# Performance work log

Hardware: AMD Instinct MI355X
Metric: run time of the kernel (lower is better)

Reference implementation:

```python
import jax, jax.numpy as jnp
import numpy as np

B, X, Y, Z = 1, 256, 256, 48
N_LABELS = 40  # static instance count (labels 1..N_LABELS; 0 = background)


def setup_inputs() -> dict:
    key = jax.random.key(0)
    # watershed integer label volume [B, 1, X, Y, Z]; stored as float32 (labels are
    # small non-negative integers, faithful to torch mask semantics under equality)
    mask = jax.random.randint(key, (B, 1, X, Y, Z), 0, N_LABELS + 1).astype(jnp.float32)
    return {"mask": mask, "n_labels": N_LABELS}


def reference(mask, n_labels):
    """Vectorized _colormask_to_mask: [B,1,X,Y,Z] int labels -> [B,N,X,Y,Z] one-hot.

    The torch original loops over each unique nonzero label u and writes
    out[:, i] = (mask == u). With labels known to be 1..n_labels, this is a
    single broadcasted equality (one-pass scatter-style expansion), removing
    the O(N) Python loop over full-volume comparisons.
    """
    labels = jnp.arange(1, n_labels + 1, dtype=mask.dtype).reshape(1, -1, 1, 1, 1)
    # [B,1,X,Y,Z] == [1,N,1,1,1] -> [B,N,X,Y,Z]
    return (mask == labels).astype(jnp.float32)
```

## Files before the change

kernel.cpp:

```cpp
#include <hip/hip_runtime.h>
#include <hip/hip_bf16.h>


constexpr int V = 256 * 256 * 48;
constexpr int N_LABELS = 40;

typedef float f32x4 __attribute__((ext_vector_type(4)));

__global__ __launch_bounds__(256)
void onehot_kernel(const float* __restrict__ mask, float* __restrict__ out) {
    const int i = (blockIdx.x * blockDim.x + threadIdx.x) * 4;
    const int n = blockIdx.y;
    const float lab = (float)(n + 1);

    const f32x4 m = *reinterpret_cast<const f32x4*>(mask + i);

    f32x4 o;
    o.x = (m.x == lab) ? 1.0f : 0.0f;
    o.y = (m.y == lab) ? 1.0f : 0.0f;
    o.z = (m.z == lab) ? 1.0f : 0.0f;
    o.w = (m.w == lab) ? 1.0f : 0.0f;

    __builtin_nontemporal_store(o, reinterpret_cast<f32x4*>(out + (size_t)n * V + i));
}

extern "C" void kernel_launch(void* const* d_in, const int* in_sizes, int n_in,
                              void* d_out, int out_size, void* d_ws, size_t ws_size,
                              hipStream_t stream) {
    const float* mask = (const float*)d_in[0];
    float* out = (float*)d_out;

    const int threads = 256;
    const int blocks_x = (V / 4) / threads;
    dim3 grid(blocks_x, N_LABELS);

    onehot_kernel<<<grid, threads, 0, stream>>>(mask, out);
}
```

Before: 477.2 us.

## Load mask once per thread and loop over all labels in-kernel

Each thread now loads 16 mask values into registers once and writes all 40 label planes from them, instead of one block per label re-reading the mask. This cuts mask reads from 40 passes to one and leaves 768 blocks, each doing 160 stores. The nontemporal store hint is also dropped in favour of plain stores, which may change cache behaviour for the 503 MB output write.

```diff
diff --git a/kernel.cpp b/kernel.cpp
--- a/kernel.cpp
+++ b/kernel.cpp
@@ -4,24 +4,35 @@
 
 constexpr int V = 256 * 256 * 48;
 constexpr int N_LABELS = 40;
+constexpr int TPB = 256;
+constexpr int VPT = 16;
+constexpr int CHUNK = TPB * VPT;
 
 typedef float f32x4 __attribute__((ext_vector_type(4)));
 
-__global__ __launch_bounds__(256)
+__global__ __launch_bounds__(TPB)
 void onehot_kernel(const float* __restrict__ mask, float* __restrict__ out) {
-    const int i = (blockIdx.x * blockDim.x + threadIdx.x) * 4;
-    const int n = blockIdx.y;
-    const float lab = (float)(n + 1);
+    const int base = blockIdx.x * CHUNK;
+    const int toff = threadIdx.x * 4;
 
-    const f32x4 m = *reinterpret_cast<const f32x4*>(mask + i);
+    f32x4 m[4];
+#pragma unroll
+    for (int k = 0; k < 4; ++k)
+        m[k] = *reinterpret_cast<const f32x4*>(mask + base + k * (TPB * 4) + toff);
 
-    f32x4 o;
-    o.x = (m.x == lab) ? 1.0f : 0.0f;
-    o.y = (m.y == lab) ? 1.0f : 0.0f;
-    o.z = (m.z == lab) ? 1.0f : 0.0f;
-    o.w = (m.w == lab) ? 1.0f : 0.0f;
-
-    __builtin_nontemporal_store(o, reinterpret_cast<f32x4*>(out + (size_t)n * V + i));
+    for (int n = 0; n < N_LABELS; ++n) {
+        const float lab = (float)(n + 1);
+        float* op = out + (size_t)n * V + base + toff;
+#pragma unroll
+        for (int k = 0; k < 4; ++k) {
+            f32x4 o;
+            o.x = (m[k].x == lab) ? 1.0f : 0.0f;
+            o.y = (m[k].y == lab) ? 1.0f : 0.0f;
+            o.z = (m[k].z == lab) ? 1.0f : 0.0f;
+            o.w = (m[k].w == lab) ? 1.0f : 0.0f;
+            *reinterpret_cast<f32x4*>(op + k * (TPB * 4)) = o;
+        }
+    }
 }
 
 extern "C" void kernel_launch(void* const* d_in, const int* in_sizes, int n_in,
@@ -30,9 +41,7 @@
     const float* mask = (const float*)d_in[0];
     float* out = (float*)d_out;
 
-    const int threads = 256;
-    const int blocks_x = (V / 4) / threads;
-    dim3 grid(blocks_x, N_LABELS);
+    dim3 grid(V / CHUNK);
 
-    onehot_kernel<<<grid, threads, 0, stream>>>(mask, out);
+    onehot_kernel<<<grid, TPB, 0, stream>>>(mask, out);
 }
```

Result: slower. 489.9 us (+2.7%).
